# Kernel tuning notes

Hardware: AMD Instinct MI355X
Metric: run time of the kernel (lower is better)

## Reference

```python
import jax, jax.numpy as jnp
import numpy as np

G, N, D, H = 2, 192, 64, 4
DK = D // H


def setup_inputs() -> dict:
    key = jax.random.key(0)
    ks = jax.random.split(key, 9)
    s = 0.05
    return {
        "adj": jax.random.normal(ks[0], (G, N, N, D), dtype=jnp.float32),
        "Wq": jax.random.normal(ks[1], (D, D), dtype=jnp.float32) * s,
        "bq": jax.random.normal(ks[2], (D,), dtype=jnp.float32) * s,
        "Wk": jax.random.normal(ks[3], (D, D), dtype=jnp.float32) * s,
        "bk": jax.random.normal(ks[4], (D,), dtype=jnp.float32) * s,
        "Wv": jax.random.normal(ks[5], (D, D), dtype=jnp.float32) * s,
        "bv": jax.random.normal(ks[6], (D,), dtype=jnp.float32) * s,
        "Wo": jax.random.normal(ks[7], (D, D), dtype=jnp.float32) * s,
        "bo": jax.random.normal(ks[8], (D,), dtype=jnp.float32) * s,
    }


def _proj_heads(x, W, b):
    # x: (G,N,N,D) -> (G,N,H,N,DK); W stored as (in,out)
    y = jnp.einsum('gnmd,de->gnme', x, W) + b
    g, n, m, _ = y.shape
    return y.reshape(g, n, m, H, DK).transpose(0, 1, 3, 2, 4)


def reference(adj, Wq, bq, Wk, bk, Wv, bv, Wo, bo):
    q = _proj_heads(adj, Wq, bq)  # (G,N,H,N,DK)
    k = _proj_heads(adj, Wk, bk)
    v = _proj_heads(adj, Wv, bv)
    scores = jnp.einsum('gnhtd,gnhsd->gnhts', q, k) / jnp.sqrt(jnp.float32(DK))
    p = jax.nn.softmax(scores, axis=-1)  # (G,N,H,N,N)
    x = jnp.einsum('gnhts,gnhsd->gnhtd', p, v)  # (G,N,H,N,DK)
    x = x.transpose(0, 1, 3, 2, 4).reshape(adj.shape[0], adj.shape[1], -1, H * DK)
    return jnp.einsum('gnmd,de->gnme', x, Wo) + bo
```

## Files before the change

### kernel.cpp

```cpp
#include <hip/hip_runtime.h>


typedef float    f32x4 __attribute__((ext_vector_type(4)));
typedef _Float16 f16x4 __attribute__((ext_vector_type(4)));
typedef _Float16 f16x8 __attribute__((ext_vector_type(8)));

__device__ __forceinline__ int xsw64(int r, int c) {
    return (r << 6) + (((c >> 3) ^ (r & 7)) << 3) + (c & 7);
}
__device__ __forceinline__ int qsw64(int r, int c) {
    return (r << 6) + (((c >> 2) ^ (r & 15)) << 2) + (c & 3);
}
__device__ __forceinline__ int vsw192(int r, int c) {
    return r * 192 + ((((c >> 3) ^ (r & 7)) & 31) << 3) + (c & 7);
}

extern "C" __global__ void __launch_bounds__(512, 1)
spa_mfma(const float* __restrict__ adj,
         const float* __restrict__ Wq, const float* __restrict__ bq,
         const float* __restrict__ Wk, const float* __restrict__ bk,
         const float* __restrict__ Wv, const float* __restrict__ bv,
         const float* __restrict__ Wo, const float* __restrict__ bo,
         float* __restrict__ out) {
    extern __shared__ __align__(16) char smem[];
    _Float16* X  = (_Float16*)smem;
    _Float16* Qs = (_Float16*)smem + 12288;
    _Float16* Ks = (_Float16*)smem + 24576;
    _Float16* VT = (_Float16*)smem + 36864;
    _Float16* XA = (_Float16*)smem + 49152;
    _Float16* WT = (_Float16*)smem + 61440;

    const int tid = threadIdx.x;
    const int l   = tid & 63;
    const int wv  = tid >> 6;
    const int l15 = l & 15;
    const int g   = l >> 4;

    const float* Xg   = adj + (size_t)blockIdx.x * (192 * 64);
    float*       outg = out + (size_t)blockIdx.x * (192 * 64);

    {
        const int d0 = (tid & 7) << 3;
        const int t0 = tid >> 3;
        for (int p = 0; p < 3; ++p) {
            int t = t0 + (p << 6);
            const float4* src = (const float4*)&Xg[(t << 6) + d0];
            float4 v0 = src[0], v1 = src[1];
            f16x8 h8;
            h8[0] = (_Float16)v0.x; h8[1] = (_Float16)v0.y;
            h8[2] = (_Float16)v0.z; h8[3] = (_Float16)v0.w;
            h8[4] = (_Float16)v1.x; h8[5] = (_Float16)v1.y;
            h8[6] = (_Float16)v1.z; h8[7] = (_Float16)v1.w;
            *(f16x8*)&X[xsw64(t, d0)] = h8;
        }
    }
    {
        const int e  = tid & 63;
        const int db = (tid >> 6) << 3;
        const float* Ws[4] = {Wq, Wk, Wv, Wo};
#pragma unroll
        for (int m = 0; m < 4; ++m) {
            f16x8 h8;
#pragma unroll
            for (int j = 0; j < 8; ++j) h8[j] = (_Float16)Ws[m][(db + j) * 64 + e];
            *(f16x8*)&WT[m * 4096 + xsw64(e, db)] = h8;
        }
    }
    __syncthreads();

    const f32x4 z = {0.f, 0.f, 0.f, 0.f};

    if (wv < 4) {
        const int e = (wv << 4) + l15;
        f16x8 wq0 = *(const f16x8*)&WT[0 * 4096 + xsw64(e, (g << 3))];
        f16x8 wq1 = *(const f16x8*)&WT[0 * 4096 + xsw64(e, 32 + (g << 3))];
        f16x8 wk0 = *(const f16x8*)&WT[1 * 4096 + xsw64(e, (g << 3))];
        f16x8 wk1 = *(const f16x8*)&WT[1 * 4096 + xsw64(e, 32 + (g << 3))];
        const float bqv = bq[e], bkv = bk[e];
        for (int tt = 0; tt < 12; ++tt) {
            f16x8 x0 = *(const f16x8*)&X[xsw64((tt << 4) + l15, (g << 3))];
            f16x8 x1 = *(const f16x8*)&X[xsw64((tt << 4) + l15, 32 + (g << 3))];
            f32x4 aq = __builtin_amdgcn_mfma_f32_16x16x32_f16(x0, wq0, z, 0, 0, 0);
            aq = __builtin_amdgcn_mfma_f32_16x16x32_f16(x1, wq1, aq, 0, 0, 0);
            f32x4 ak = __builtin_amdgcn_mfma_f32_16x16x32_f16(x0, wk0, z, 0, 0, 0);
            ak = __builtin_amdgcn_mfma_f32_16x16x32_f16(x1, wk1, ak, 0, 0, 0);
#pragma unroll
            for (int r = 0; r < 4; ++r) {
                int t = (tt << 4) + (g << 2) + r;
                Qs[qsw64(t, e)] = (_Float16)((aq[r] + bqv) * 0.25f);
                Ks[qsw64(t, e)] = (_Float16)(ak[r] + bkv);
            }
        }
    } else {
        const int et = wv - 4;
        const int er = (et << 4) + l15;
        f16x8 wv0 = *(const f16x8*)&WT[2 * 4096 + xsw64(er, (g << 3))];
        f16x8 wv1 = *(const f16x8*)&WT[2 * 4096 + xsw64(er, 32 + (g << 3))];
        float bvv[4];
#pragma unroll
        for (int r = 0; r < 4; ++r) bvv[r] = bv[(et << 4) + (g << 2) + r];
        for (int st = 0; st < 12; ++st) {
            f16x8 x0 = *(const f16x8*)&X[xsw64((st << 4) + l15, (g << 3))];
            f16x8 x1 = *(const f16x8*)&X[xsw64((st << 4) + l15, 32 + (g << 3))];
            f32x4 av_ = __builtin_amdgcn_mfma_f32_16x16x32_f16(wv0, x0, z, 0, 0, 0);
            av_ = __builtin_amdgcn_mfma_f32_16x16x32_f16(wv1, x1, av_, 0, 0, 0);
            const int s = (st << 4) + l15;
#pragma unroll
            for (int r = 0; r < 4; ++r) {
                int e2 = (et << 4) + (g << 2) + r;
                VT[vsw192(e2, s)] = (_Float16)(av_[r] + bvv[r]);
            }
        }
    }
    __syncthreads();

    {
        const int h  = wv >> 1;
        const int eh = h << 4;
        f16x4 kf[12], vf[12];
#pragma unroll
        for (int st = 0; st < 12; ++st) {
            kf[st] = *(const f16x4*)&Ks[qsw64((st << 4) + l15, eh + (g << 2))];
            vf[st] = *(const f16x4*)&VT[vsw192(eh + l15, (st << 4) + (g << 2))];
        }
        for (int j = 0; j < 6; ++j) {
            const int tb = (((wv & 1) * 6 + j) << 4);
            f16x4 qf = *(const f16x4*)&Qs[qsw64(tb + l15, eh + (g << 2))];
            f32x4 accA = z, accB = z;
            float rsum = 0.f;
#pragma unroll
            for (int st = 0; st < 12; ++st) {
                f32x4 c = __builtin_amdgcn_mfma_f32_16x16x16f16(kf[st], qf, z, 0, 0, 0);
                float p0 = __expf(c[0]), p1 = __expf(c[1]);
                float p2 = __expf(c[2]), p3 = __expf(c[3]);
                rsum += (p0 + p1) + (p2 + p3);
                f16x4 pf;
                pf[0] = (_Float16)p0; pf[1] = (_Float16)p1;
                pf[2] = (_Float16)p2; pf[3] = (_Float16)p3;
                if (st & 1) accB = __builtin_amdgcn_mfma_f32_16x16x16f16(vf[st], pf, accB, 0, 0, 0);
                else        accA = __builtin_amdgcn_mfma_f32_16x16x16f16(vf[st], pf, accA, 0, 0, 0);
            }
            rsum += __shfl_xor(rsum, 16);
            rsum += __shfl_xor(rsum, 32);
            const float rinv = 1.0f / rsum;
            f16x4 o4;
#pragma unroll
            for (int r = 0; r < 4; ++r) o4[r] = (_Float16)((accA[r] + accB[r]) * rinv);
            const int t = tb + l15;
            *(f16x4*)&XA[xsw64(t, eh + (g << 2))] = o4;
        }
    }
    __syncthreads();

    {
        const int eo = ((wv & 3) << 4) + l15;
        f16x8 wo0 = *(const f16x8*)&WT[3 * 4096 + xsw64(eo, (g << 3))];
        f16x8 wo1 = *(const f16x8*)&WT[3 * 4096 + xsw64(eo, 32 + (g << 3))];
        const float bov = bo[eo];
        for (int i = 0; i < 6; ++i) {
            const int tt = (wv + (i << 3)) >> 2;
            f16x8 a0 = *(const f16x8*)&XA[xsw64((tt << 4) + l15, (g << 3))];
            f16x8 a1 = *(const f16x8*)&XA[xsw64((tt << 4) + l15, 32 + (g << 3))];
            f32x4 acc = __builtin_amdgcn_mfma_f32_16x16x32_f16(a0, wo0, z, 0, 0, 0);
            acc = __builtin_amdgcn_mfma_f32_16x16x32_f16(a1, wo1, acc, 0, 0, 0);
#pragma unroll
            for (int r = 0; r < 4; ++r) {
                int t = (tt << 4) + (g << 2) + r;
                outg[(t << 6) + eo] = acc[r] + bov;
            }
        }
    }
}

extern "C" void kernel_launch(void* const* d_in, const int* in_sizes, int n_in,
                              void* d_out, int out_size, void* d_ws, size_t ws_size,
                              hipStream_t stream) {
    (void)in_sizes; (void)n_in; (void)d_ws; (void)ws_size; (void)out_size;
    const float* adj = (const float*)d_in[0];
    const float* Wq  = (const float*)d_in[1];
    const float* bq  = (const float*)d_in[2];
    const float* Wk  = (const float*)d_in[3];
    const float* bk  = (const float*)d_in[4];
    const float* Wv  = (const float*)d_in[5];
    const float* bv  = (const float*)d_in[6];
    const float* Wo  = (const float*)d_in[7];
    const float* bo  = (const float*)d_in[8];
    float* out = (float*)d_out;

    const int shmem = 155648;
    hipFuncSetAttribute((const void*)spa_mfma,
                        hipFuncAttributeMaxDynamicSharedMemorySize, shmem);
    spa_mfma<<<2 * 192, 512, shmem, stream>>>(adj, Wq, bq, Wk, bk, Wv, bv, Wo, bo, out);
}
```

Measured before the change: 105.9 us.

## Keep Q/K projections in registers and shrink LDS to fit two blocks per CU

Q and K projections are now computed per wave directly into MFMA fragment registers instead of being staged in shared memory. The attention output reuses the input X buffer, which cuts dynamic LDS from about 152KB to 80KB so more blocks can be resident per CU. exp is replaced with exp2, with log2e folded into the Q scale. In exchange, K is computed twice (each of two waves per head computes its own copy), and launch bounds now request 4 blocks, which constrains registers and may cause spills.

```diff
diff --git a/kernel.cpp b/kernel.cpp
--- a/kernel.cpp
+++ b/kernel.cpp
@@ -8,27 +8,21 @@
 __device__ __forceinline__ int xsw64(int r, int c) {
     return (r << 6) + (((c >> 3) ^ (r & 7)) << 3) + (c & 7);
 }
-__device__ __forceinline__ int qsw64(int r, int c) {
-    return (r << 6) + (((c >> 2) ^ (r & 15)) << 2) + (c & 3);
-}
 __device__ __forceinline__ int vsw192(int r, int c) {
     return r * 192 + ((((c >> 3) ^ (r & 7)) & 31) << 3) + (c & 7);
 }
 
-extern "C" __global__ void __launch_bounds__(512, 1)
-spa_mfma(const float* __restrict__ adj,
-         const float* __restrict__ Wq, const float* __restrict__ bq,
-         const float* __restrict__ Wk, const float* __restrict__ bk,
-         const float* __restrict__ Wv, const float* __restrict__ bv,
-         const float* __restrict__ Wo, const float* __restrict__ bo,
-         float* __restrict__ out) {
+extern "C" __global__ void __launch_bounds__(512, 4)
+spa_mfma2(const float* __restrict__ adj,
+          const float* __restrict__ Wq, const float* __restrict__ bq,
+          const float* __restrict__ Wk, const float* __restrict__ bk,
+          const float* __restrict__ Wv, const float* __restrict__ bv,
+          const float* __restrict__ Wo, const float* __restrict__ bo,
+          float* __restrict__ out) {
     extern __shared__ __align__(16) char smem[];
     _Float16* X  = (_Float16*)smem;
-    _Float16* Qs = (_Float16*)smem + 12288;
-    _Float16* Ks = (_Float16*)smem + 24576;
-    _Float16* VT = (_Float16*)smem + 36864;
-    _Float16* XA = (_Float16*)smem + 49152;
-    _Float16* WT = (_Float16*)smem + 61440;
+    _Float16* VT = (_Float16*)smem + 12288;
+    _Float16* WT = (_Float16*)smem + 24576;
 
     const int tid = threadIdx.x;
     const int l   = tid & 63;
@@ -47,10 +41,8 @@
             const float4* src = (const float4*)&Xg[(t << 6) + d0];
             float4 v0 = src[0], v1 = src[1];
             f16x8 h8;
-            h8[0] = (_Float16)v0.x; h8[1] = (_Float16)v0.y;
-            h8[2] = (_Float16)v0.z; h8[3] = (_Float16)v0.w;
-            h8[4] = (_Float16)v1.x; h8[5] = (_Float16)v1.y;
-            h8[6] = (_Float16)v1.z; h8[7] = (_Float16)v1.w;
+            h8[0]=(_Float16)v0.x; h8[1]=(_Float16)v0.y; h8[2]=(_Float16)v0.z; h8[3]=(_Float16)v0.w;
+            h8[4]=(_Float16)v1.x; h8[5]=(_Float16)v1.y; h8[6]=(_Float16)v1.z; h8[7]=(_Float16)v1.w;
             *(f16x8*)&X[xsw64(t, d0)] = h8;
         }
     }
@@ -69,105 +61,108 @@
     __syncthreads();
 
     const f32x4 z = {0.f, 0.f, 0.f, 0.f};
+    const int h  = wv >> 1;
+    const int eh = h << 4;
 
-    if (wv < 4) {
-        const int e = (wv << 4) + l15;
-        f16x8 wq0 = *(const f16x8*)&WT[0 * 4096 + xsw64(e, (g << 3))];
-        f16x8 wq1 = *(const f16x8*)&WT[0 * 4096 + xsw64(e, 32 + (g << 3))];
-        f16x8 wk0 = *(const f16x8*)&WT[1 * 4096 + xsw64(e, (g << 3))];
-        f16x8 wk1 = *(const f16x8*)&WT[1 * 4096 + xsw64(e, 32 + (g << 3))];
-        const float bqv = bq[e], bkv = bk[e];
-        for (int tt = 0; tt < 12; ++tt) {
-            f16x8 x0 = *(const f16x8*)&X[xsw64((tt << 4) + l15, (g << 3))];
-            f16x8 x1 = *(const f16x8*)&X[xsw64((tt << 4) + l15, 32 + (g << 3))];
-            f32x4 aq = __builtin_amdgcn_mfma_f32_16x16x32_f16(x0, wq0, z, 0, 0, 0);
-            aq = __builtin_amdgcn_mfma_f32_16x16x32_f16(x1, wq1, aq, 0, 0, 0);
-            f32x4 ak = __builtin_amdgcn_mfma_f32_16x16x32_f16(x0, wk0, z, 0, 0, 0);
-            ak = __builtin_amdgcn_mfma_f32_16x16x32_f16(x1, wk1, ak, 0, 0, 0);
+    {
+        const int et  = wv & 3;
+        const int stb = (wv >> 2) * 6;
+        f16x8 w0 = *(const f16x8*)&WT[2*4096 + xsw64((et<<4)+l15, g<<3)];
+        f16x8 w1 = *(const f16x8*)&WT[2*4096 + xsw64((et<<4)+l15, 32+(g<<3))];
+        f32x4 b4 = *(const f32x4*)&bv[(et<<4)+(g<<2)];
+        for (int s6 = 0; s6 < 6; ++s6) {
+            int st = stb + s6;
+            f16x8 x0 = *(const f16x8*)&X[xsw64((st<<4)+l15, g<<3)];
+            f16x8 x1 = *(const f16x8*)&X[xsw64((st<<4)+l15, 32+(g<<3))];
+            f32x4 c = __builtin_amdgcn_mfma_f32_16x16x32_f16(w0, x0, z, 0,0,0);
+            c = __builtin_amdgcn_mfma_f32_16x16x32_f16(w1, x1, c, 0,0,0);
+            int s = (st << 4) + l15;
 #pragma unroll
-            for (int r = 0; r < 4; ++r) {
-                int t = (tt << 4) + (g << 2) + r;
-                Qs[qsw64(t, e)] = (_Float16)((aq[r] + bqv) * 0.25f);
-                Ks[qsw64(t, e)] = (_Float16)(ak[r] + bkv);
-            }
+            for (int r = 0; r < 4; ++r)
+                VT[vsw192((et<<4)+(g<<2)+r, s)] = (_Float16)(c[r] + b4[r]);
         }
-    } else {
-        const int et = wv - 4;
-        const int er = (et << 4) + l15;
-        f16x8 wv0 = *(const f16x8*)&WT[2 * 4096 + xsw64(er, (g << 3))];
-        f16x8 wv1 = *(const f16x8*)&WT[2 * 4096 + xsw64(er, 32 + (g << 3))];
-        float bvv[4];
+    }
+
+    f16x4 kf[12];
+    {
+        f16x8 w0 = *(const f16x8*)&WT[1*4096 + xsw64(eh+l15, g<<3)];
+        f16x8 w1 = *(const f16x8*)&WT[1*4096 + xsw64(eh+l15, 32+(g<<3))];
+        f32x4 b4 = *(const f32x4*)&bk[eh+(g<<2)];
 #pragma unroll
-        for (int r = 0; r < 4; ++r) bvv[r] = bv[(et << 4) + (g << 2) + r];
         for (int st = 0; st < 12; ++st) {
-            f16x8 x0 = *(const f16x8*)&X[xsw64((st << 4) + l15, (g << 3))];
-            f16x8 x1 = *(const f16x8*)&X[xsw64((st << 4) + l15, 32 + (g << 3))];
-            f32x4 av_ = __builtin_amdgcn_mfma_f32_16x16x32_f16(wv0, x0, z, 0, 0, 0);
-            av_ = __builtin_amdgcn_mfma_f32_16x16x32_f16(wv1, x1, av_, 0, 0, 0);
-            const int s = (st << 4) + l15;
+            f16x8 x0 = *(const f16x8*)&X[xsw64((st<<4)+l15, g<<3)];
+            f16x8 x1 = *(const f16x8*)&X[xsw64((st<<4)+l15, 32+(g<<3))];
+            f32x4 c = __builtin_amdgcn_mfma_f32_16x16x32_f16(w0, x0, z, 0,0,0);
+            c = __builtin_amdgcn_mfma_f32_16x16x32_f16(w1, x1, c, 0,0,0);
 #pragma unroll
-            for (int r = 0; r < 4; ++r) {
-                int e2 = (et << 4) + (g << 2) + r;
-                VT[vsw192(e2, s)] = (_Float16)(av_[r] + bvv[r]);
-            }
+            for (int r = 0; r < 4; ++r) kf[st][r] = (_Float16)(c[r] + b4[r]);
+        }
+    }
+
+    f16x4 qf[6];
+    const int ttb = (wv & 1) * 6;
+    {
+        f16x8 w0 = *(const f16x8*)&WT[0*4096 + xsw64(eh+l15, g<<3)];
+        f16x8 w1 = *(const f16x8*)&WT[0*4096 + xsw64(eh+l15, 32+(g<<3))];
+        f32x4 b4 = *(const f32x4*)&bq[eh+(g<<2)];
+        const float qs = 0.25f * 1.4426950408889634f;
+#pragma unroll
+        for (int j = 0; j < 6; ++j) {
+            int tt = ttb + j;
+            f16x8 x0 = *(const f16x8*)&X[xsw64((tt<<4)+l15, g<<3)];
+            f16x8 x1 = *(const f16x8*)&X[xsw64((tt<<4)+l15, 32+(g<<3))];
+            f32x4 c = __builtin_amdgcn_mfma_f32_16x16x32_f16(w0, x0, z, 0,0,0);
+            c = __builtin_amdgcn_mfma_f32_16x16x32_f16(w1, x1, c, 0,0,0);
+#pragma unroll
+            for (int r = 0; r < 4; ++r) qf[j][r] = (_Float16)((c[r] + b4[r]) * qs);
         }
     }
     __syncthreads();
 
-    {
-        const int h  = wv >> 1;
-        const int eh = h << 4;
-        f16x4 kf[12], vf[12];
+    f16x4 vf[12];
+#pragma unroll
+    for (int st = 0; st < 12; ++st)
+        vf[st] = *(const f16x4*)&VT[vsw192(eh+l15, (st<<4)+(g<<2))];
+
+    for (int j = 0; j < 6; ++j) {
+        f32x4 accA = z, accB = z;
+        float rsum = 0.f;
 #pragma unroll
         for (int st = 0; st < 12; ++st) {
-            kf[st] = *(const f16x4*)&Ks[qsw64((st << 4) + l15, eh + (g << 2))];
-            vf[st] = *(const f16x4*)&VT[vsw192(eh + l15, (st << 4) + (g << 2))];
+            f32x4 c = __builtin_amdgcn_mfma_f32_16x16x16f16(kf[st], qf[j], z, 0,0,0);
+            float p0 = exp2f(c[0]), p1 = exp2f(c[1]);
+            float p2 = exp2f(c[2]), p3 = exp2f(c[3]);
+            rsum += (p0 + p1) + (p2 + p3);
+            f16x4 pf;
+            pf[0]=(_Float16)p0; pf[1]=(_Float16)p1; pf[2]=(_Float16)p2; pf[3]=(_Float16)p3;
+            if (st & 1) accB = __builtin_amdgcn_mfma_f32_16x16x16f16(vf[st], pf, accB, 0,0,0);
+            else        accA = __builtin_amdgcn_mfma_f32_16x16x16f16(vf[st], pf, accA, 0,0,0);
         }
-        for (int j = 0; j < 6; ++j) {
-            const int tb = (((wv & 1) * 6 + j) << 4);
-            f16x4 qf = *(const f16x4*)&Qs[qsw64(tb + l15, eh + (g << 2))];
-            f32x4 accA = z, accB = z;
-            float rsum = 0.f;
+        rsum += __shfl_xor(rsum, 16);
+        rsum += __shfl_xor(rsum, 32);
+        const float rinv = 1.0f / rsum;
+        f16x4 o4;
 #pragma unroll
-            for (int st = 0; st < 12; ++st) {
-                f32x4 c = __builtin_amdgcn_mfma_f32_16x16x16f16(kf[st], qf, z, 0, 0, 0);
-                float p0 = __expf(c[0]), p1 = __expf(c[1]);
-                float p2 = __expf(c[2]), p3 = __expf(c[3]);
-                rsum += (p0 + p1) + (p2 + p3);
-                f16x4 pf;
-                pf[0] = (_Float16)p0; pf[1] = (_Float16)p1;
-                pf[2] = (_Float16)p2; pf[3] = (_Float16)p3;
-                if (st & 1) accB = __builtin_amdgcn_mfma_f32_16x16x16f16(vf[st], pf, accB, 0, 0, 0);
-                else        accA = __builtin_amdgcn_mfma_f32_16x16x16f16(vf[st], pf, accA, 0, 0, 0);
-            }
-            rsum += __shfl_xor(rsum, 16);
-            rsum += __shfl_xor(rsum, 32);
-            const float rinv = 1.0f / rsum;
-            f16x4 o4;
-#pragma unroll
-            for (int r = 0; r < 4; ++r) o4[r] = (_Float16)((accA[r] + accB[r]) * rinv);
-            const int t = tb + l15;
-            *(f16x4*)&XA[xsw64(t, eh + (g << 2))] = o4;
-        }
+        for (int r = 0; r < 4; ++r) o4[r] = (_Float16)((accA[r] + accB[r]) * rinv);
+        *(f16x4*)&X[xsw64(((ttb + j) << 4) + l15, eh + (g << 2))] = o4;
     }
     __syncthreads();
 
     {
         const int eo = ((wv & 3) << 4) + l15;
-        f16x8 wo0 = *(const f16x8*)&WT[3 * 4096 + xsw64(eo, (g << 3))];
-        f16x8 wo1 = *(const f16x8*)&WT[3 * 4096 + xsw64(eo, 32 + (g << 3))];
+        f16x8 w0 = *(const f16x8*)&WT[3*4096 + xsw64(eo, g<<3)];
+        f16x8 w1 = *(const f16x8*)&WT[3*4096 + xsw64(eo, 32+(g<<3))];
         const float bov = bo[eo];
+#pragma unroll
         for (int i = 0; i < 6; ++i) {
-            const int tt = (wv + (i << 3)) >> 2;
-            f16x8 a0 = *(const f16x8*)&XA[xsw64((tt << 4) + l15, (g << 3))];
-            f16x8 a1 = *(const f16x8*)&XA[xsw64((tt << 4) + l15, 32 + (g << 3))];
-            f32x4 acc = __builtin_amdgcn_mfma_f32_16x16x32_f16(a0, wo0, z, 0, 0, 0);
-            acc = __builtin_amdgcn_mfma_f32_16x16x32_f16(a1, wo1, acc, 0, 0, 0);
+            int tt = (wv + (i << 3)) >> 2;
+            f16x8 a0 = *(const f16x8*)&X[xsw64((tt<<4)+l15, g<<3)];
+            f16x8 a1 = *(const f16x8*)&X[xsw64((tt<<4)+l15, 32+(g<<3))];
+            f32x4 c = __builtin_amdgcn_mfma_f32_16x16x32_f16(a0, w0, z, 0,0,0);
+            c = __builtin_amdgcn_mfma_f32_16x16x32_f16(a1, w1, c, 0,0,0);
 #pragma unroll
-            for (int r = 0; r < 4; ++r) {
-                int t = (tt << 4) + (g << 2) + r;
-                outg[(t << 6) + eo] = acc[r] + bov;
-            }
+            for (int r = 0; r < 4; ++r)
+                outg[(((tt << 4) + (g << 2) + r) << 6) + eo] = c[r] + bov;
         }
     }
 }
@@ -187,8 +182,8 @@
     const float* bo  = (const float*)d_in[8];
     float* out = (float*)d_out;
 
-    const int shmem = 155648;
-    hipFuncSetAttribute((const void*)spa_mfma,
+    const int shmem = 81920;
+    hipFuncSetAttribute((const void*)spa_mfma2,
                         hipFuncAttributeMaxDynamicSharedMemorySize, shmem);
-    spa_mfma<<<2 * 192, 512, shmem, stream>>>(adj, Wq, bq, Wk, bk, Wv, bv, Wo, bo, out);
+    spa_mfma2<<<2 * 192, 512, shmem, stream>>>(adj, Wq, bq, Wk, bk, Wv, bv, Wo, bo, out);
 }
```

New measurement: 110.4 us. +4.2%, slower.
